# Kernel tuning notes

Hardware: AMD Instinct MI355X
Metric: run time of the kernel (lower is better)

The kernel has to match this reference:

```python
import jax, jax.numpy as jnp
import numpy as np

N = 20000        # number of graph nodes (objects + regions)
E = 660000       # number of directed edges (~avg degree 33)
F_DIM = 254      # feature_dims = in_feats // 2
IN_FEATS = 508   # (256 - 2) * 2
GLOVE = 300


def _gcn_layer(x, W, b, src, dst, norm_src, norm_dst):
    """DGL GraphConv, norm='both'. W: [in, out], b: [out]."""
    n = x.shape[0]
    pre_mult = W.shape[0] > W.shape[1]  # DGL applies W first if in > out
    if pre_mult:
        x = x @ W
    h = (x * norm_src[:, None])[src]                      # [E, F] gather
    agg = jax.ops.segment_sum(h, dst, num_segments=n)     # scatter-add [N, F]
    agg = agg * norm_dst[:, None]
    if not pre_mult:
        agg = agg @ W
    return agg + b


def setup_inputs() -> dict:
    key = jax.random.key(0)
    ks = jax.random.split(key, 12)
    w = lambda k, shape: jax.random.normal(k, shape, jnp.float32) * 0.02
    return {
        "class_embed": jax.random.normal(ks[0], (N,), jnp.float32),
        "all_glove": jax.random.normal(ks[1], (N, GLOVE), jnp.float32),
        "W_word": w(ks[2], (F_DIM, GLOVE)),
        "b_word": jnp.zeros((F_DIM,), jnp.float32),
        "W_img": w(ks[3], (F_DIM, N)),
        "b_img": jnp.zeros((F_DIM,), jnp.float32),
        "W1": w(ks[4], (IN_FEATS, IN_FEATS)),
        "b1": jnp.zeros((IN_FEATS,), jnp.float32),
        "W2": w(ks[5], (IN_FEATS, IN_FEATS)),
        "b2": jnp.zeros((IN_FEATS,), jnp.float32),
        "W3": w(ks[6], (IN_FEATS, 1)),
        "b3": jnp.zeros((1,), jnp.float32),
        "W_fin": w(ks[7], (F_DIM, N)),
        "b_fin": jnp.zeros((F_DIM,), jnp.float32),
        "src": jax.random.randint(ks[8], (E,), 0, N, jnp.int32),
        "dst": jax.random.randint(ks[9], (E,), 0, N, jnp.int32),
    }


def reference(class_embed, all_glove, W_word, b_word, W_img, b_img,
              W1, b1, W2, b2, W3, b3, W_fin, b_fin, src, dst):
    n = all_glove.shape[0]
    ones = jnp.ones(src.shape, jnp.float32)
    deg_out = jax.ops.segment_sum(ones, src, num_segments=n)
    deg_in = jax.ops.segment_sum(ones, dst, num_segments=n)
    # norm='both': zero where degree is zero (DGL replaces inf with 0)
    norm_src = jnp.where(deg_out > 0, jnp.maximum(deg_out, 1.0) ** -0.5, 0.0)
    norm_dst = jnp.where(deg_in > 0, jnp.maximum(deg_in, 1.0) ** -0.5, 0.0)

    ce = class_embed.reshape(1, -1) @ W_img.T + b_img      # [1, 254]
    we = all_glove @ W_word.T + b_word                     # [N, 254]
    x = jnp.concatenate([jnp.broadcast_to(ce, (n, F_DIM)), we], axis=1)  # [N, 508]

    h = jax.nn.relu(_gcn_layer(x, W1, b1, src, dst, norm_src, norm_dst))
    h = jax.nn.relu(_gcn_layer(h, W2, b2, src, dst, norm_src, norm_dst))
    o = jax.nn.relu(_gcn_layer(h, W3, b3, src, dst, norm_src, norm_dst))  # [N, 1]

    return o.reshape(1, -1) @ W_fin.T + b_fin              # [1, 254]
```

## Files before the change

### kernel.cpp

```cpp
#include <hip/hip_runtime.h>
#include <hip/hip_bf16.h>

#define TPB 256
#define NB_E 32
#define HTPB 512
#define NHALF_LDS 10240

typedef __attribute__((ext_vector_type(8))) short bf16x8_t;
typedef __attribute__((ext_vector_type(4))) float f32x4_t;
typedef __attribute__((ext_vector_type(8))) unsigned short u16x8_t;
typedef __attribute__((ext_vector_type(4))) unsigned short u16x4_t;

__device__ __forceinline__ float bf2f(unsigned short u) {
    return __uint_as_float(((unsigned)u) << 16);
}
__device__ __forceinline__ unsigned short f2bf(float f) {
    unsigned x = __float_as_uint(f);
    unsigned r = (x + 0x7fff + ((x >> 16) & 1)) >> 16;
    return (unsigned short)r;
}


__global__ __launch_bounds__(HTPB) void hist_kernel(
    const int* __restrict__ src, const int* __restrict__ dst,
    int* __restrict__ histD, int* __restrict__ histS,
    int E, int N, int nhalf, int chunk) {
    __shared__ int h[NHALF_LDS];
    int b = blockIdx.x, var = blockIdx.y;
    const int* arr = (var < 2) ? dst : src;
    int lo = (var & 1) * nhalf;
    int hi = min(lo + nhalf, N);
    int cnt = hi - lo;
    for (int i = threadIdx.x; i < cnt; i += HTPB) h[i] = 0;
    __syncthreads();
    int beg = b * chunk, end = min(E, beg + chunk);
    for (int i = beg + threadIdx.x; i < end; i += HTPB) {
        int v = arr[i];
        if (v >= lo && v < hi) atomicAdd(&h[v - lo], 1);
    }
    __syncthreads();
    int* out = ((var < 2) ? histD : histS) + (size_t)b * N + lo;
    for (int i = threadIdx.x; i < cnt; i += HTPB) out[i] = h[i];
}

__global__ void degreduce_kernel(const int* __restrict__ histD, const int* __restrict__ histS,
                                 float* __restrict__ ns, float* __restrict__ nd,
                                 int* __restrict__ degp, int N) {
    int n = blockIdx.x * blockDim.x + threadIdx.x;
    if (n >= N) return;
    int di = 0, dout = 0;
    for (int b = 0; b < NB_E; b++) {
        di += histD[(size_t)b * N + n];
        dout += histS[(size_t)b * N + n];
    }
    nd[n] = di > 0 ? rsqrtf((float)di) : 0.f;
    ns[n] = dout > 0 ? rsqrtf((float)dout) : 0.f;
    degp[n] = (di + 7) & ~7;
}

__global__ __launch_bounds__(1024) void scan1(const int* __restrict__ degp,
                                              int* __restrict__ rp, int* __restrict__ bsum, int n) {
    __shared__ int buf[1024];
    int b = blockIdx.x;
    int i = b * 1024 + threadIdx.x;
    int v = (i < n) ? degp[i] : 0;
    buf[threadIdx.x] = v;
    __syncthreads();
    for (int off = 1; off < 1024; off <<= 1) {
        int t = (threadIdx.x >= off) ? buf[threadIdx.x - off] : 0;
        __syncthreads();
        buf[threadIdx.x] += t;
        __syncthreads();
    }
    if (i < n) rp[i + 1] = buf[threadIdx.x];
    if (threadIdx.x == 1023) bsum[b] = buf[1023];
    if (b == 0 && threadIdx.x == 0) rp[0] = 0;
}

__global__ void scan2(int* __restrict__ bsum, int nb) {
    int lane = threadIdx.x;
    int v = (lane < nb) ? bsum[lane] : 0;
    for (int off = 1; off < 64; off <<= 1) {
        int t = __shfl_up(v, off);
        if (lane >= off) v += t;
    }
    if (lane < nb) bsum[lane] = v;
}

__global__ __launch_bounds__(1024) void scan3(int* __restrict__ rp, const int* __restrict__ bsum, int n) {
    int b = blockIdx.x;
    if (b == 0) return;
    int i = b * 1024 + threadIdx.x;
    if (i < n) rp[i + 1] += bsum[b - 1];
}

__global__ void gbase_kernel(const int* __restrict__ histD, const int* __restrict__ rp,
                             int* __restrict__ gbase, int N) {
    int n = blockIdx.x * blockDim.x + threadIdx.x;
    if (n >= N) return;
    int run = rp[n];
    for (int b = 0; b < NB_E; b++) {
        gbase[(size_t)b * N + n] = run;
        run += histD[(size_t)b * N + n];
    }
}

__global__ __launch_bounds__(HTPB) void scatter2_kernel(
    const int* __restrict__ src, const int* __restrict__ dst,
    const int* __restrict__ gbase, const float* __restrict__ ns,
    int2* __restrict__ payload, int E, int N, int nhalf, int chunk) {
    __shared__ int h[NHALF_LDS];
    int b = blockIdx.x, half = blockIdx.y;
    int lo = half * nhalf;
    int hi = min(lo + nhalf, N);
    int cnt = hi - lo;
    for (int i = threadIdx.x; i < cnt; i += HTPB) h[i] = 0;
    __syncthreads();
    int beg = b * chunk, end = min(E, beg + chunk);
    for (int i = beg + threadIdx.x; i < end; i += HTPB) {
        int d = dst[i];
        if (d >= lo && d < hi) {
            int s = src[i];
            int rank = atomicAdd(&h[d - lo], 1);
            int pos = gbase[(size_t)b * N + d] + rank;
            payload[pos] = make_int2(s, __float_as_int(ns[s]));
        }
    }
}

__global__ __launch_bounds__(256) void st_kernel(const int* __restrict__ rp,
                                                 const int2* __restrict__ payload,
                                                 const float* __restrict__ nd,
                                                 float* __restrict__ tv, int n) {
    int d = blockIdx.x * 4 + (threadIdx.x >> 6);
    if (d >= n) return;
    int lane = threadIdx.x & 63;
    int beg = rp[d], end = rp[d + 1];
    float acc = 0.f;
    for (int e = beg + lane; e < end; e += 64) acc += __int_as_float(payload[e].y);
    for (int off = 32; off > 0; off >>= 1) acc += __shfl_down(acc, off);
    if (lane == 0) tv[d] = acc * nd[d];
}


__global__ void gemv_rows(const float* __restrict__ vec, const float* __restrict__ Mat,
                          const float* __restrict__ bias, float* __restrict__ out, int n) {
    int j = blockIdx.x;
    const float* row = Mat + (size_t)j * n;
    float s = 0.f;
    for (int i = threadIdx.x; i < n; i += blockDim.x) s += vec[i] * row[i];
    __shared__ float red[TPB];
    red[threadIdx.x] = s;
    __syncthreads();
    for (int o = TPB / 2; o > 0; o >>= 1) {
        if (threadIdx.x < o) red[threadIdx.x] += red[threadIdx.x + o];
        __syncthreads();
    }
    if (threadIdx.x == 0) out[j] = red[0] + (bias ? bias[j] : 0.f);
}

__global__ __launch_bounds__(64) void u_kernel(const float* __restrict__ ce, const float* __restrict__ W1,
                                               float* __restrict__ u, int FD, int IF) {
    int j = blockIdx.x;
    int lane = threadIdx.x;
    float s = 0.f;
    for (int i = lane; i < FD; i += 64) s += ce[i] * W1[(size_t)i * IF + j];
    for (int off = 32; off > 0; off >>= 1) s += __shfl_down(s, off);
    if (lane == 0) u[j] = s;
}


__global__ void pad_convert4(const float* __restrict__ in, int icols, int irows,
                             unsigned short* __restrict__ out, int ocols, int orows, int cpr) {
    int idx = blockIdx.x * blockDim.x + threadIdx.x;
    int row = idx / cpr;
    int c4 = (idx - row * cpr) * 4;
    if (row >= orows) return;
    float4 v = make_float4(0.f, 0.f, 0.f, 0.f);
    if (row < irows && c4 < icols)
        v = *(const float4*)(in + (size_t)row * icols + c4);
    u16x4_t o;
    o[0] = f2bf(v.x); o[1] = f2bf(v.y); o[2] = f2bf(v.z); o[3] = f2bf(v.w);
    *(u16x4_t*)(out + (size_t)row * ocols + c4) = o;
}

__global__ void transpose_pad(const float* __restrict__ W, int rows, int cols, int ldw,
                              unsigned short* __restrict__ out, int orows, int ocols) {
    __shared__ float tile[32][33];
    int k0 = blockIdx.x * 32, n0 = blockIdx.y * 32;
    int tx = threadIdx.x, ty = threadIdx.y;
    for (int i = 0; i < 32; i += 8) {
        int k = k0 + ty + i, n = n0 + tx;
        tile[ty + i][tx] = (k < rows && n < cols) ? W[(size_t)k * ldw + n] : 0.f;
    }
    __syncthreads();
    for (int i = 0; i < 32; i += 8) {
        int n = n0 + ty + i, k = k0 + tx;
        if (n < orows && k < ocols) out[(size_t)n * ocols + k] = f2bf(tile[tx][ty + i]);
    }
}

__global__ __launch_bounds__(256) void mfma_gemm(
    const unsigned short* __restrict__ A, const unsigned short* __restrict__ Bt,
    const float* __restrict__ bias, const float* __restrict__ rowscale,
    const float* __restrict__ tvec, const float* __restrict__ uvec,
    const float* __restrict__ w3, float* __restrict__ zout,
    unsigned short* __restrict__ C, int M, int Nn, int Kp, int Cld, int relu) {
    __shared__ unsigned short As[128 * 32];
    __shared__ unsigned short Bs[128 * 32];
    int tid = threadIdx.x;
    int lane = tid & 63;
    int wave = tid >> 6;
    int wm = wave >> 1, wn = wave & 1;
    int lg = lane >> 4, lt = lane & 15;
    int row0 = blockIdx.y * 128, col0 = blockIdx.x * 128;

    f32x4_t acc[4][4] = {};

    int nk = Kp >> 5;
    for (int kp = 0; kp < nk; kp++) {
        int k0 = kp << 5;
#pragma unroll
        for (int i = 0; i < 2; i++) {
            int cid = tid + i * 256;
            int r = cid >> 2, c = cid & 3;
            int sw = c ^ ((r >> 1) & 3);
            int4 av = make_int4(0, 0, 0, 0);
            int grA = row0 + r;
            if (grA < M) av = *(const int4*)(A + (size_t)grA * Kp + k0 + (c << 3));
            *(int4*)(As + r * 32 + sw * 8) = av;
            int4 bv = *(const int4*)(Bt + (size_t)(col0 + r) * Kp + k0 + (c << 3));
            *(int4*)(Bs + r * 32 + sw * 8) = bv;
        }
        __syncthreads();
        bf16x8_t af[4], bfr[4];
#pragma unroll
        for (int mi = 0; mi < 4; mi++) {
            int r = wm * 64 + mi * 16 + lt;
            int sw = lg ^ ((r >> 1) & 3);
            af[mi] = *(const bf16x8_t*)(As + r * 32 + sw * 8);
        }
#pragma unroll
        for (int ni = 0; ni < 4; ni++) {
            int r = wn * 64 + ni * 16 + lt;
            int sw = lg ^ ((r >> 1) & 3);
            bfr[ni] = *(const bf16x8_t*)(Bs + r * 32 + sw * 8);
        }
#pragma unroll
        for (int mi = 0; mi < 4; mi++)
#pragma unroll
            for (int ni = 0; ni < 4; ni++)
                acc[mi][ni] = __builtin_amdgcn_mfma_f32_16x16x32_bf16(af[mi], bfr[ni], acc[mi][ni], 0, 0, 0);
        __syncthreads();
    }

#pragma unroll
    for (int mi = 0; mi < 4; mi++) {
#pragma unroll
        for (int r = 0; r < 4; r++) {
            int row = row0 + wm * 64 + mi * 16 + lg * 4 + r;
            if (row >= M) continue;
            float rs = rowscale ? rowscale[row] : 1.f;
            float tvr = tvec ? tvec[row] : 0.f;
            float zp = 0.f;
#pragma unroll
            for (int ni = 0; ni < 4; ni++) {
                int colb = col0 + wn * 64 + ni * 16 + lt;
                float v = 0.f;
                if (colb < Nn) {
                    v = acc[mi][ni][r] * rs;
                    if (bias) v += bias[colb];
                    if (tvec) v += tvr * uvec[colb];
                    if (relu) v = fmaxf(v, 0.f);
                    if (w3) zp += v * w3[colb];
                }
                if (C) C[(size_t)row * Cld + colb] = f2bf(v);
            }
            if (w3) {
                zp += __shfl_xor(zp, 1);
                zp += __shfl_xor(zp, 2);
                zp += __shfl_xor(zp, 4);
                zp += __shfl_xor(zp, 8);
                if (lt == 0) atomicAdd(&zout[row], zp);
            }
        }
    }
}

__global__ __launch_bounds__(256) void spmm_bf16_cols(
    const int* __restrict__ rp, const int2* __restrict__ payload,
    const unsigned short* __restrict__ X, unsigned short* __restrict__ Y,
    int n, int ld, int c0) {
    int node = blockIdx.x * 4 + (threadIdx.x >> 6);
    if (node >= n) return;
    int lane = threadIdx.x & 63;
    const unsigned short* Xo = X + c0 + lane * 4;
    int beg = rp[node], end = rp[node + 1];
    float acc[4] = {};
    for (int e = beg; e < end; e += 8) {
        int2 p[8];
#pragma unroll
        for (int j = 0; j < 8; j++) p[j] = payload[e + j];
        u16x4_t v[8];
#pragma unroll
        for (int j = 0; j < 8; j++) v[j] = *(const u16x4_t*)(Xo + (size_t)p[j].x * ld);
#pragma unroll
        for (int j = 0; j < 8; j++) {
            float w = __int_as_float(p[j].y);
#pragma unroll
            for (int c = 0; c < 4; c++) acc[c] += w * bf2f(v[j][c]);
        }
    }
    u16x4_t o;
#pragma unroll
    for (int c = 0; c < 4; c++) o[c] = f2bf(acc[c]);
    *(u16x4_t*)(Y + (size_t)node * ld + c0 + lane * 4) = o;
}


__global__ __launch_bounds__(256) void z_gather(const int* __restrict__ rp,
                                                const int2* __restrict__ payload,
                                                const float* __restrict__ z,
                                                const float* __restrict__ nd, const float* __restrict__ b3,
                                                float* __restrict__ o, int n) {
    int d = blockIdx.x * 4 + (threadIdx.x >> 6);
    if (d >= n) return;
    int lane = threadIdx.x & 63;
    int beg = rp[d], end = rp[d + 1];
    float acc = 0.f;
    for (int e = beg + lane; e < end; e += 64) {
        int2 p = payload[e];
        acc += __int_as_float(p.y) * z[p.x];
    }
    for (int off = 32; off > 0; off >>= 1) acc += __shfl_down(acc, off);
    if (lane == 0) o[d] = fmaxf(nd[d] * acc + b3[0], 0.f);
}


extern "C" void kernel_launch(void* const* d_in, const int* in_sizes, int n_in,
                              void* d_out, int out_size, void* d_ws, size_t ws_size,
                              hipStream_t stream) {
    const float* class_embed = (const float*)d_in[0];
    const float* all_glove   = (const float*)d_in[1];
    const float* W_word = (const float*)d_in[2];
    const float* b_word = (const float*)d_in[3];
    const float* W_img  = (const float*)d_in[4];
    const float* b_img  = (const float*)d_in[5];
    const float* W1 = (const float*)d_in[6];
    const float* b1 = (const float*)d_in[7];
    const float* W2 = (const float*)d_in[8];
    const float* b2 = (const float*)d_in[9];
    const float* W3 = (const float*)d_in[10];
    const float* b3 = (const float*)d_in[11];
    const float* W_fin = (const float*)d_in[12];
    const float* b_fin = (const float*)d_in[13];
    const int* src = (const int*)d_in[14];
    const int* dst = (const int*)d_in[15];

    const int N   = in_sizes[0];
    const int GLV = in_sizes[1] / N;
    const int FD  = in_sizes[5];
    const int IF  = in_sizes[7];
    const int E   = in_sizes[14];

    const int GLVp = 320;
    const int FDp  = 256;
    const int IFp  = 512;
    const int EP   = E + 8 * N;
    const int nhalf = (N + 1) / 2;
    const int chunk = (E + NB_E - 1) / NB_E;

    char* base = (char*)d_ws;
    size_t off = 0;
    auto alloc = [&](size_t bytes) -> void* {
        void* p = base + off;
        off = (off + bytes + 255) & ~(size_t)255;
        return p;
    };

    float* ns  = (float*)alloc((size_t)N * 4);
    float* nd  = (float*)alloc((size_t)N * 4);
    float* z   = (float*)alloc((size_t)N * 4);
    float* tv  = (float*)alloc((size_t)N * 4);
    float* ce  = (float*)alloc((size_t)FD * 4);
    float* u   = (float*)alloc((size_t)IF * 4);
    float* ov  = (float*)alloc((size_t)N * 4);
    int* degp  = (int*)alloc((size_t)N * 4);
    int* rp    = (int*)alloc((size_t)(N + 1) * 4);
    int* bsum  = (int*)alloc(64 * 4);
    int* histD = (int*)alloc((size_t)NB_E * N * 4);
    int* histS = (int*)alloc((size_t)NB_E * N * 4);
    int* gbase = (int*)alloc((size_t)NB_E * N * 4);
    int2* payload = (int2*)alloc((size_t)EP * 8);
    unsigned short* WwP  = (unsigned short*)alloc((size_t)FDp * GLVp * 2);
    unsigned short* W1hT = (unsigned short*)alloc((size_t)IFp * FDp * 2);
    unsigned short* W2T  = (unsigned short*)alloc((size_t)IFp * IFp * 2);
    unsigned short* glove_bf = (unsigned short*)alloc((size_t)N * GLVp * 2);
    unsigned short* we       = (unsigned short*)alloc((size_t)N * FDp * 2);
    unsigned short* h12      = (unsigned short*)alloc((size_t)N * IFp * 2);
    unsigned short* aggwe = glove_bf;
    unsigned short* agg2  = glove_bf;
    unsigned short* h1 = h12;

    hipMemsetAsync(z, 0, (size_t)N * 4, stream);
    hipMemsetAsync(payload, 0, (size_t)EP * 8, stream);

    int gN = (N + TPB - 1) / TPB;
    int nb = (N + 1023) / 1024;

    {
        dim3 g(NB_E, 4);
        hist_kernel<<<g, HTPB, 0, stream>>>(src, dst, histD, histS, E, N, nhalf, chunk);
    }
    degreduce_kernel<<<gN, TPB, 0, stream>>>(histD, histS, ns, nd, degp, N);
    scan1<<<nb, 1024, 0, stream>>>(degp, rp, bsum, N);
    scan2<<<1, 64, 0, stream>>>(bsum, nb);
    scan3<<<nb, 1024, 0, stream>>>(rp, bsum, N);
    gbase_kernel<<<gN, TPB, 0, stream>>>(histD, rp, gbase, N);
    {
        dim3 g(NB_E, 2);
        scatter2_kernel<<<g, HTPB, 0, stream>>>(src, dst, gbase, ns, payload, E, N, nhalf, chunk);
    }
    st_kernel<<<(N + 3) / 4, 256, 0, stream>>>(rp, payload, nd, tv, N);

    gemv_rows<<<FD, TPB, 0, stream>>>(class_embed, W_img, b_img, ce, N);
    u_kernel<<<IF, 64, 0, stream>>>(ce, W1, u, FD, IF);

    {
        int cpr = GLVp / 4;
        int tot = N * cpr;
        pad_convert4<<<(tot + 255) / 256, 256, 0, stream>>>(all_glove, GLV, N, glove_bf, GLVp, N, cpr);
        int tot2 = FDp * cpr;
        pad_convert4<<<(tot2 + 255) / 256, 256, 0, stream>>>(W_word, GLV, FD, WwP, GLVp, FDp, cpr);
    }
    {
        dim3 g(FDp / 32, IFp / 32);
        transpose_pad<<<g, dim3(32, 8), 0, stream>>>(W1 + (size_t)FD * IF, FD, IF, IF, W1hT, IFp, FDp);
    }
    {
        dim3 g(IFp / 32, IFp / 32);
        transpose_pad<<<g, dim3(32, 8), 0, stream>>>(W2, IF, IF, IF, W2T, IFp, IFp);
    }

    int mtiles = (N + 127) / 128;

    {
        dim3 g(FDp / 128, mtiles);
        mfma_gemm<<<g, 256, 0, stream>>>(glove_bf, WwP, b_word, nullptr, nullptr, nullptr,
                                         nullptr, nullptr, we, N, FD, GLVp, FDp, 0);
    }
    spmm_bf16_cols<<<(N + 3) / 4, 256, 0, stream>>>(rp, payload, we, aggwe, N, FDp, 0);
    {
        dim3 g(IFp / 128, mtiles);
        mfma_gemm<<<g, 256, 0, stream>>>(aggwe, W1hT, b1, nd, tv, u,
                                         nullptr, nullptr, h1, N, IF, FDp, IFp, 1);
    }
    spmm_bf16_cols<<<(N + 3) / 4, 256, 0, stream>>>(rp, payload, h1, agg2, N, IFp, 0);
    spmm_bf16_cols<<<(N + 3) / 4, 256, 0, stream>>>(rp, payload, h1, agg2, N, IFp, 256);
    {
        dim3 g(IFp / 128, mtiles);
        mfma_gemm<<<g, 256, 0, stream>>>(agg2, W2T, b2, nd, nullptr, nullptr,
                                         W3, z, nullptr, N, IF, IFp, IFp, 1);
    }
    z_gather<<<(N + 3) / 4, 256, 0, stream>>>(rp, payload, z, nd, b3, ov, N);
    gemv_rows<<<FD, TPB, 0, stream>>>(ov, W_fin, b_fin, (float*)d_out, N);
}
```

Before: 381.3 us.

## Use direct global-to-LDS loads and XCD-aware tile remap in MFMA GEMM

The GEMM tile loads now use global_load_lds to move 16-byte chunks straight into LDS, skipping the register round-trip. The source-side swizzle keeps the bank-conflict layout the MFMA reads expect. Workgroup IDs are remapped so consecutive tiles land on the same XCD, which should improve L2 reuse. Row buffers are padded to a multiple of 128 so the bounds check on A rows can be dropped. The catch is that aggwe/agg2/h1 alias padded buffers whose tail rows may hold stale data; this is harmless unless it is read into valid outputs.

New measurement: 376.7 us. No clear change (-1.2%).

```diff
diff --git a/kernel.cpp b/kernel.cpp
--- a/kernel.cpp
+++ b/kernel.cpp
@@ -18,6 +18,12 @@
     unsigned x = __float_as_uint(f);
     unsigned r = (x + 0x7fff + ((x >> 16) & 1)) >> 16;
     return (unsigned short)r;
+}
+
+__device__ __forceinline__ void gload16(const unsigned short* g, unsigned short* l) {
+    __builtin_amdgcn_global_load_lds(
+        (const __attribute__((address_space(1))) unsigned int*)(const void*)g,
+        (__attribute__((address_space(3))) unsigned int*)(void*)l, 16, 0, 0);
 }
 
 
@@ -213,7 +219,13 @@
     int wave = tid >> 6;
     int wm = wave >> 1, wn = wave & 1;
     int lg = lane >> 4, lt = lane & 15;
-    int row0 = blockIdx.y * 128, col0 = blockIdx.x * 128;
+
+    int nwg = gridDim.x * gridDim.y;
+    int hid = blockIdx.y * gridDim.x + blockIdx.x;
+    int q = nwg >> 3, r8 = nwg & 7;
+    int xcd = hid & 7, pos = hid >> 3;
+    int wg = (xcd < r8 ? xcd * (q + 1) : r8 * (q + 1) + (xcd - r8) * q) + pos;
+    int row0 = (wg / gridDim.x) * 128, col0 = (wg % gridDim.x) * 128;
 
     f32x4_t acc[4][4] = {};
 
@@ -225,12 +237,8 @@
             int cid = tid + i * 256;
             int r = cid >> 2, c = cid & 3;
             int sw = c ^ ((r >> 1) & 3);
-            int4 av = make_int4(0, 0, 0, 0);
-            int grA = row0 + r;
-            if (grA < M) av = *(const int4*)(A + (size_t)grA * Kp + k0 + (c << 3));
-            *(int4*)(As + r * 32 + sw * 8) = av;
-            int4 bv = *(const int4*)(Bt + (size_t)(col0 + r) * Kp + k0 + (c << 3));
-            *(int4*)(Bs + r * 32 + sw * 8) = bv;
+            gload16(A + (size_t)(row0 + r) * Kp + k0 + (sw << 3), As + cid * 8);
+            gload16(Bt + (size_t)(col0 + r) * Kp + k0 + (sw << 3), Bs + cid * 8);
         }
         __syncthreads();
         bf16x8_t af[4], bfr[4];
@@ -366,6 +374,7 @@
     const int GLVp = 320;
     const int FDp  = 256;
     const int IFp  = 512;
+    const int Mp   = (N + 127) & ~127;
     const int EP   = E + 8 * N;
     const int nhalf = (N + 1) / 2;
     const int chunk = (E + NB_E - 1) / NB_E;
@@ -395,9 +404,9 @@
     unsigned short* WwP  = (unsigned short*)alloc((size_t)FDp * GLVp * 2);
     unsigned short* W1hT = (unsigned short*)alloc((size_t)IFp * FDp * 2);
     unsigned short* W2T  = (unsigned short*)alloc((size_t)IFp * IFp * 2);
-    unsigned short* glove_bf = (unsigned short*)alloc((size_t)N * GLVp * 2);
-    unsigned short* we       = (unsigned short*)alloc((size_t)N * FDp * 2);
-    unsigned short* h12      = (unsigned short*)alloc((size_t)N * IFp * 2);
+    unsigned short* glove_bf = (unsigned short*)alloc((size_t)Mp * GLVp * 2);
+    unsigned short* we       = (unsigned short*)alloc((size_t)Mp * FDp * 2);
+    unsigned short* h12      = (unsigned short*)alloc((size_t)Mp * IFp * 2);
     unsigned short* aggwe = glove_bf;
     unsigned short* agg2  = glove_bf;
     unsigned short* h1 = h12;
@@ -428,8 +437,8 @@
 
     {
         int cpr = GLVp / 4;
-        int tot = N * cpr;
-        pad_convert4<<<(tot + 255) / 256, 256, 0, stream>>>(all_glove, GLV, N, glove_bf, GLVp, N, cpr);
+        int tot = Mp * cpr;
+        pad_convert4<<<(tot + 255) / 256, 256, 0, stream>>>(all_glove, GLV, N, glove_bf, GLVp, Mp, cpr);
         int tot2 = FDp * cpr;
         pad_convert4<<<(tot2 + 255) / 256, 256, 0, stream>>>(W_word, GLV, FD, WwP, GLVp, FDp, cpr);
     }
@@ -442,7 +451,7 @@
         transpose_pad<<<g, dim3(32, 8), 0, stream>>>(W2, IF, IF, IF, W2T, IFp, IFp);
     }
 
-    int mtiles = (N + 127) / 128;
+    int mtiles = Mp / 128;
 
     {
         dim3 g(FDp / 128, mtiles);
```
